# Optimization experiments

Hardware: AMD Instinct MI355X
Metric: run time of the kernel (lower is better)

## Reference

```python
import jax, jax.numpy as jnp
import numpy as np

B, S, H = 4, 2048, 576
NH, NKV, HD = 9, 3, 64
NEG = -1e9


def rotate_half(x):
    x1, x2 = x[..., : HD // 2], x[..., HD // 2 :]
    return jnp.concatenate((-x2, x1), axis=-1)


def setup_inputs() -> dict:
    key = jax.random.key(0)
    ks = jax.random.split(key, 6)
    x = jax.random.normal(ks[0], (B, S, H), dtype=jnp.float32)
    # realistic RoPE tables
    inv_freq = 1.0 / (10000.0 ** (np.arange(0, HD, 2, dtype=np.float32) / HD))
    pos = np.arange(S, dtype=np.float32)
    freqs = np.outer(pos, inv_freq)            # [S, HD//2]
    emb = np.concatenate([freqs, freqs], -1)   # [S, HD]
    cos = jnp.asarray(np.cos(emb), dtype=jnp.float32)
    sin = jnp.asarray(np.sin(emb), dtype=jnp.float32)
    # causal additive mask [1,1,S,S]
    causal = jnp.tril(jnp.ones((S, S), dtype=jnp.bool_))
    mask = jnp.where(causal, 0.0, NEG).astype(jnp.float32)[None, None]
    sc = 1.0 / np.sqrt(H)
    Wq = jax.random.normal(ks[1], (H, NH * HD), dtype=jnp.float32) * sc
    Wk = jax.random.normal(ks[2], (H, NKV * HD), dtype=jnp.float32) * sc
    Wv = jax.random.normal(ks[3], (H, NKV * HD), dtype=jnp.float32) * sc
    Wo = jax.random.normal(ks[4], (NH * HD, H), dtype=jnp.float32) * sc
    return {"x": x, "cos": cos, "sin": sin, "mask": mask,
            "Wq": Wq, "Wk": Wk, "Wv": Wv, "Wo": Wo}


def reference(x, cos, sin, mask, Wq, Wk, Wv, Wo):
    b, s, _ = x.shape
    # projections -> [b, heads, s, hd]
    q = (x @ Wq).reshape(b, s, NH, HD).transpose(0, 2, 1, 3)
    k = (x @ Wk).reshape(b, s, NKV, HD).transpose(0, 2, 1, 3)
    v = (x @ Wv).reshape(b, s, NKV, HD).transpose(0, 2, 1, 3)
    c = cos[None, None]  # [1,1,s,hd]
    sn = sin[None, None]
    q = q * c + rotate_half(q) * sn
    k = k * c + rotate_half(k) * sn
    # GQA: repeat_interleave KV heads to match query heads
    groups = NH // NKV
    k = jnp.repeat(k, groups, axis=1)
    v = jnp.repeat(v, groups, axis=1)
    scores = jnp.einsum("bhqd,bhkd->bhqk", q, k) / np.sqrt(HD)
    scores = scores + mask
    probs = jax.nn.softmax(scores, axis=-1)
    out = jnp.einsum("bhqk,bhkd->bhqd", probs, v)
    out = out.transpose(0, 2, 1, 3).reshape(b, s, NH * HD)
    return out @ Wo
```

## Files before the change

### kernel.cpp

```cpp
#include <hip/hip_runtime.h>
#include <math.h>

typedef __attribute__((ext_vector_type(4))) float f32x4;
typedef __attribute__((ext_vector_type(8))) short short8;
typedef __attribute__((ext_vector_type(8))) __bf16 bf16x8;
typedef __attribute__((ext_vector_type(2))) __bf16 bf16x2;
typedef __attribute__((ext_vector_type(2))) unsigned uint32x2;

#define NB 4
#define NS 2048
#define NHID 576
#define NHEADS 9
#define NKVH 3
#define NHD 64
#define NM (NB * NS)
#define NQKV 960
#define QKS 768
#define NGRP 3
#define QSC 0.18033688f

static __device__ __forceinline__ unsigned short f2bf(float f) {
  union { float f; unsigned u; } v; v.f = f;
  unsigned r = v.u + 0x7FFFu + ((v.u >> 16) & 1u);
  return (unsigned short)(r >> 16);
}
static __device__ __forceinline__ unsigned pk2bf(float a, float b) {
  bf16x2 h;
  h.x = (__bf16)a;
  h.y = (__bf16)b;
  return __builtin_bit_cast(unsigned, h);
}
static __device__ __forceinline__ float bf2f(unsigned short h) {
  union { unsigned u; float f; } v; v.u = ((unsigned)h) << 16;
  return v.f;
}
static __device__ __forceinline__ float fexp2(float x) {
  return __builtin_amdgcn_exp2f(x);
}
static __device__ __forceinline__ f32x4 mfma16(short8 a, short8 b, f32x4 c) {
  return __builtin_amdgcn_mfma_f32_16x16x32_bf16(
      __builtin_bit_cast(bf16x8, a), __builtin_bit_cast(bf16x8, b), c, 0, 0, 0);
}
static __device__ __forceinline__ void gload16(const void* g, void* l) {
  __builtin_amdgcn_global_load_lds(
      (const __attribute__((address_space(1))) void*)g,
      (__attribute__((address_space(3))) void*)l, 16, 0, 0);
}

__global__ __launch_bounds__(256)
void k_prep(const float* __restrict__ x, unsigned short* __restrict__ xb,
            const float* __restrict__ Wq, const float* __restrict__ Wk,
            const float* __restrict__ Wv, const float* __restrict__ Wo,
            unsigned short* __restrict__ wqkvT, unsigned short* __restrict__ woT) {
  __shared__ unsigned short tile[64 * 72];
  int bid = blockIdx.x;
  if (bid < 2304) {
    const int t = bid * 256 + threadIdx.x;
    const f32x4* sp = (const f32x4*)(x + (size_t)t * 8);
    f32x4 a = sp[0], b = sp[1];
    union { short8 v; unsigned short u[8]; } o;
#pragma unroll
    for (int e = 0; e < 4; ++e) { o.u[e] = f2bf(a[e]); o.u[4 + e] = f2bf(b[e]); }
    *(short8*)(xb + (size_t)t * 8) = o.v;
    return;
  }
  bid -= 2304;
  const float* src;
  unsigned short* dst;
  int C, bx, by;
  if (bid < 81) { src = Wq; dst = wqkvT; C = 576; bx = bid % 9; by = bid / 9; }
  else if (bid < 108) { int b2 = bid - 81; src = Wk; dst = wqkvT + 576 * 576; C = 192; bx = b2 % 3; by = b2 / 3; }
  else if (bid < 135) { int b2 = bid - 108; src = Wv; dst = wqkvT + 768 * 576; C = 192; bx = b2 % 3; by = b2 / 3; }
  else { int b2 = bid - 135; src = Wo; dst = woT; C = 576; bx = b2 % 9; by = b2 / 9; }
  const int R = 576;
  const int t = threadIdx.x;
  const int r0 = by * 64, c0 = bx * 64;
  {
    const int rl = t >> 2, cb = (t & 3) * 16;
    const float* sp = src + (size_t)(r0 + rl) * C + c0 + cb;
#pragma unroll
    for (int jj = 0; jj < 4; ++jj) {
      f32x4 v = *(const f32x4*)(sp + jj * 4);
#pragma unroll
      for (int e = 0; e < 4; ++e) tile[rl * 72 + cb + jj * 4 + e] = f2bf(v[e]);
    }
  }
  __syncthreads();
  {
    const int cl = t >> 2, rb = (t & 3) * 16;
    union { short8 v; unsigned short u[8]; } o0, o1;
#pragma unroll
    for (int jj = 0; jj < 8; ++jj) {
      o0.u[jj] = tile[(rb + jj) * 72 + cl];
      o1.u[jj] = tile[(rb + 8 + jj) * 72 + cl];
    }
    unsigned short* dp = dst + (size_t)(c0 + cl) * R + r0 + rb;
    *(short8*)dp = o0.v;
    *(short8*)(dp + 8) = o1.v;
  }
}

template <int MODE>
__global__ __launch_bounds__(256)
void k_gemm_bt(const unsigned short* __restrict__ A,
               const unsigned short* __restrict__ Bt,
               void* __restrict__ Cv,
               unsigned short* __restrict__ vtb,
               const float* __restrict__ cosT,
               const float* __restrict__ sinT,
               const int M, const int N, const int K) {
  __shared__ unsigned short a_lds[2][128 * 64];
  __shared__ unsigned short b_lds[2][128 * 64];
  const int tid = threadIdx.x;
  const int w = tid >> 6, l = tid & 63, g = l >> 4, c = l & 15;
  const int tm = blockIdx.y * 128, tn = blockIdx.x * 128;
  const int wm = w >> 1, wn = w & 1;
  f32x4 acc[4][4] = {};
  const int nk = K >> 6;

#define GSTAGE(k0, half)                                                   \
  {                                                                        \
    _Pragma("unroll")                                                      \
    for (int q = 0; q < 4; ++q) {                                          \
      const int o = q * 4096 + w * 1024 + l * 16;                          \
      const int row = o >> 7;                                              \
      const int wb = (o & 127) ^ ((row & 7) << 4);                         \
      gload16(A + (size_t)(tm + row) * K + (k0) + (wb >> 1),               \
              (void*)(a_lds[half] + ((q * 4096 + w * 1024) >> 1)));        \
      gload16(Bt + (size_t)(tn + row) * K + (k0) + (wb >> 1),              \
              (void*)(b_lds[half] + ((q * 4096 + w * 1024) >> 1)));        \
    }                                                                      \
  }

  GSTAGE(0, 0);

  for (int k = 0; k < nk; ++k) {
    if (k + 1 < nk) {
      GSTAGE((k + 1) << 6, (k + 1) & 1);
      asm volatile("s_waitcnt vmcnt(8)" ::: "memory");
    } else {
      asm volatile("s_waitcnt vmcnt(0)" ::: "memory");
    }
    __builtin_amdgcn_s_barrier();
    __builtin_amdgcn_sched_barrier(0);
    const char* al = (const char*)a_lds[k & 1];
    const char* bl = (const char*)b_lds[k & 1];
#pragma unroll
    for (int dc = 0; dc < 2; ++dc) {
      short8 af[4], bf[4];
#pragma unroll
      for (int mt = 0; mt < 4; ++mt) {
        const int row = wm * 64 + mt * 16 + c;
        const int byt = ((row << 7) + (dc << 6) + (g << 4)) ^ ((row & 7) << 4);
        af[mt] = *(const short8*)(al + byt);
      }
#pragma unroll
      for (int nt = 0; nt < 4; ++nt) {
        const int row = wn * 64 + nt * 16 + c;
        const int byt = ((row << 7) + (dc << 6) + (g << 4)) ^ ((row & 7) << 4);
        bf[nt] = *(const short8*)(bl + byt);
      }
      __builtin_amdgcn_s_setprio(1);
#pragma unroll
      for (int mt = 0; mt < 4; ++mt)
#pragma unroll
        for (int nt = 0; nt < 4; ++nt)
          acc[mt][nt] = mfma16(af[mt], bf[nt], acc[mt][nt]);
      __builtin_amdgcn_s_setprio(0);
    }
    __builtin_amdgcn_sched_barrier(0);
    __builtin_amdgcn_s_barrier();
  }
#undef GSTAGE

  if (MODE == 1) {
#pragma unroll
    for (int mt = 0; mt < 4; ++mt)
#pragma unroll
      for (int nt = 0; nt < 4; ++nt) {
        const int cc = tn + wn * 64 + nt * 16 + c;
        if (cc < N) {
#pragma unroll
          for (int i = 0; i < 4; ++i) {
            const size_t rr = (size_t)(tm + wm * 64 + mt * 16 + 4 * g + i);
            ((float*)Cv)[rr * N + cc] = acc[mt][nt][i];
          }
        }
      }
  } else if (tn < 768) {
    const float qs = (tn + wn * 64) < 576 ? QSC : 1.0f;
    unsigned short* Cp = (unsigned short*)Cv;
#pragma unroll
    for (int mt = 0; mt < 4; ++mt)
#pragma unroll
      for (int i = 0; i < 4; ++i) {
        const int rr = tm + wm * 64 + mt * 16 + 4 * g + i;
        const int s = rr & (NS - 1);
        const float* cb = cosT + (size_t)s * NHD;
        const float* sb = sinT + (size_t)s * NHD;
#pragma unroll
        for (int p = 0; p < 2; ++p) {
          const float cn = cb[p * 16 + c];
          const float sn = sb[p * 16 + c];
          const float lo = acc[mt][p][i];
          const float hi = acc[mt][p + 2][i];
          const size_t base = (size_t)rr * QKS + tn + wn * 64 + p * 16 + c;
          Cp[base] = f2bf((lo * cn - hi * sn) * qs);
          Cp[base + 32] = f2bf((hi * cn + lo * sn) * qs);
        }
      }
  } else {
#pragma unroll
    for (int mt = 0; mt < 4; ++mt)
#pragma unroll
      for (int nt = 0; nt < 4; ++nt) {
        const int cc = tn + wn * 64 + nt * 16 + c;
        if (cc < 960) {
          const int rr0 = tm + wm * 64 + mt * 16 + 4 * g;
          const int bb = rr0 >> 11, ss = rr0 & (NS - 1);
          const int grp = bb * NKVH + ((cc - 768) >> 6);
          const int d = (cc - 768) & 63;
          uint32x2 pk;
          pk.x = pk2bf(acc[mt][nt][0], acc[mt][nt][1]);
          pk.y = pk2bf(acc[mt][nt][2], acc[mt][nt][3]);
          *(uint32x2*)(vtb + (size_t)grp * (NHD * NS) + (size_t)d * NS + ss) = pk;
        }
      }
  }
}

__global__ __launch_bounds__(256)
void k_attn(const unsigned short* __restrict__ qkv,
            const unsigned short* __restrict__ vt,
            unsigned short* __restrict__ ao) {
  __shared__ unsigned short kv_s[2][2][4096];
  __shared__ unsigned short p_s[4][1024];
  const int tid = threadIdx.x;
  const int w = tid >> 6, l = tid & 63, g = l >> 4, c = l & 15;
  const int bh = blockIdx.x;
  const int qt = 31 - (int)blockIdx.y;
  const int b = bh / NHEADS, h = bh - b * NHEADS, kh = h / NGRP;

  const int lr = l >> 3;
  const int swz = ((l & 7) ^ lr) << 4;
  const int r0 = 16 * w + lr;
  const int cs = (c & 7) << 4;

  const char* kp0 = (const char*)(qkv + (size_t)b * NS * QKS + NHEADS * NHD + kh * NHD) +
                    (size_t)r0 * (QKS * 2) + swz;
  const char* kp1 = kp0 + 8 * (QKS * 2);
  const char* vp0 = (const char*)(vt + (size_t)(b * NKVH + kh) * NHD * NS) +
                    (size_t)r0 * (NS * 2) + swz;
  const char* vp1 = vp0 + 8 * (NS * 2);

  const size_t qrow = (size_t)(b * NS + qt * 64 + w * 16 + c) * QKS + h * NHD;
  const short8 qf0 = *(const short8*)(qkv + qrow + g * 8);
  const short8 qf1 = *(const short8*)(qkv + qrow + 32 + g * 8);

  const short8 ones = {0x3F80, 0x3F80, 0x3F80, 0x3F80, 0x3F80, 0x3F80, 0x3F80, 0x3F80};

  f32x4 ot[4] = {};
  f32x4 lacc = {};
  float m = -1e30f;
  const int q_g = qt * 64 + w * 16 + c;

#define STAGE(BUF)                                                \
  {                                                               \
    gload16(kp0, kv_s[BUF][0] + 16 * w * 64);                     \
    gload16(kp1, kv_s[BUF][0] + (16 * w + 8) * 64);               \
    gload16(vp0, kv_s[BUF][1] + 16 * w * 64);                     \
    gload16(vp1, kv_s[BUF][1] + (16 * w + 8) * 64);               \
    kp0 += 64 * (QKS * 2); kp1 += 64 * (QKS * 2);                 \
    vp0 += 128; vp1 += 128;                                       \
  }

#define COMPUTE(BUF, jj)                                                        \
  {                                                                             \
    const char* kl = (const char*)kv_s[BUF][0];                                 \
    const char* vl = (const char*)kv_s[BUF][1];                                 \
    f32x4 st[4] = {};                                                           \
    _Pragma("unroll")                                                           \
    for (int dc = 0; dc < 2; ++dc) {                                            \
      const int col = (dc * 64 + g * 16) ^ cs;                                  \
      const short8 qf = dc ? qf1 : qf0;                                         \
      _Pragma("unroll")                                                         \
      for (int nt = 0; nt < 4; ++nt) {                                          \
        short8 kf = *(const short8*)(kl + (nt * 16 + c) * 128 + col);           \
        st[nt] = mfma16(kf, qf, st[nt]);                                        \
      }                                                                         \
    }                                                                           \
    short8 vf[8];                                                               \
    _Pragma("unroll")                                                           \
    for (int dc = 0; dc < 2; ++dc) {                                            \
      const int col = (dc * 64 + g * 16) ^ cs;                                  \
      _Pragma("unroll")                                                         \
      for (int nt = 0; nt < 4; ++nt)                                            \
        vf[dc * 4 + nt] = *(const short8*)(vl + (nt * 16 + c) * 128 + col);     \
    }                                                                           \
    if ((jj) == qt) {                                                           \
      _Pragma("unroll")                                                         \
      for (int nt = 0; nt < 4; ++nt)                                            \
        _Pragma("unroll")                                                       \
        for (int i = 0; i < 4; ++i) {                                           \
          const int kvg = (jj) * 64 + nt * 16 + 4 * g + i;                      \
          if (kvg > q_g) st[nt][i] = -1e30f;                                    \
        }                                                                       \
    }                                                                           \
    float m0 = fmaxf(fmaxf(st[0][0], st[0][1]), st[0][2]);                      \
    float m1 = fmaxf(fmaxf(st[0][3], st[1][0]), st[1][1]);                      \
    float m2 = fmaxf(fmaxf(st[1][2], st[1][3]), st[2][0]);                      \
    float m3 = fmaxf(fmaxf(st[2][1], st[2][2]), st[2][3]);                      \
    float m4 = fmaxf(fmaxf(st[3][0], st[3][1]), st[3][2]);                      \
    float inmax = fmaxf(fmaxf(fmaxf(m0, m1), fmaxf(m2, m3)),                    \
                        fmaxf(m4, st[3][3]));                                   \
    if (!__all(inmax <= m + 8.0f)) {                                            \
      float pm = fmaxf(inmax, __shfl_xor(inmax, 16));                           \
      pm = fmaxf(pm, __shfl_xor(pm, 32));                                       \
      const float mn = fmaxf(m, pm);                                            \
      const float scl = fexp2(m - mn);                                          \
      m = mn;                                                                   \
      lacc *= scl;                                                              \
      _Pragma("unroll")                                                         \
      for (int nt = 0; nt < 4; ++nt) ot[nt] *= scl;                             \
    }                                                                           \
    {                                                                           \
      char* pw = (char*)p_s[w];                                                 \
      _Pragma("unroll")                                                         \
      for (int nt = 0; nt < 4; ++nt) {                                          \
        float p0 = fexp2(st[nt][0] - m);                                        \
        float p1 = fexp2(st[nt][1] - m);                                        \
        float p2 = fexp2(st[nt][2] - m);                                        \
        float p3 = fexp2(st[nt][3] - m);                                        \
        uint32x2 pk;                                                            \
        pk.x = pk2bf(p0, p1);                                                   \
        pk.y = pk2bf(p2, p3);                                                   \
        *(uint32x2*)(pw + c * 128 + ((nt * 32 + g * 8) ^ cs)) = pk;             \
      }                                                                         \
      _Pragma("unroll")                                                         \
      for (int dc = 0; dc < 2; ++dc) {                                          \
        const int col = (dc * 64 + g * 16) ^ cs;                                \
        short8 pf = *(const short8*)(pw + c * 128 + col);                       \
        lacc = mfma16(ones, pf, lacc);                                          \
        _Pragma("unroll")                                                       \
        for (int nt = 0; nt < 4; ++nt)                                          \
          ot[nt] = mfma16(vf[dc * 4 + nt], pf, ot[nt]);                         \
      }                                                                         \
    }                                                                           \
  }

  STAGE(0);

  for (int j = 0; j <= qt; j += 2) {
    if (j < qt) {
      STAGE(1);
      asm volatile("s_waitcnt vmcnt(4)" ::: "memory");
    } else {
      asm volatile("s_waitcnt vmcnt(0)" ::: "memory");
    }
    __builtin_amdgcn_s_barrier();
    __builtin_amdgcn_sched_barrier(0);
    COMPUTE(0, j);
    __builtin_amdgcn_sched_barrier(0);
    __builtin_amdgcn_s_barrier();
    if (j + 1 > qt) break;
    if (j + 1 < qt) {
      STAGE(0);
      asm volatile("s_waitcnt vmcnt(4)" ::: "memory");
    } else {
      asm volatile("s_waitcnt vmcnt(0)" ::: "memory");
    }
    __builtin_amdgcn_s_barrier();
    __builtin_amdgcn_sched_barrier(0);
    COMPUTE(1, j + 1);
    __builtin_amdgcn_sched_barrier(0);
    __builtin_amdgcn_s_barrier();
  }
#undef STAGE
#undef COMPUTE

  {
    char* ol = (char*)kv_s[0][0];
    const float inv = __builtin_amdgcn_rcpf(lacc[0]);
#pragma unroll
    for (int nt = 0; nt < 4; ++nt) {
      uint32x2 pk;
      pk.x = pk2bf(ot[nt][0] * inv, ot[nt][1] * inv);
      pk.y = pk2bf(ot[nt][2] * inv, ot[nt][3] * inv);
      *(uint32x2*)(ol + (w * 16 + c) * 128 + ((nt * 32 + g * 8) ^ cs)) = pk;
    }
  }
  __syncthreads();
  {
    const char* ol = (const char*)kv_s[0][0];
    const int rr = tid >> 2, cb = tid & 3;
    const int rk = (rr & 7) << 4;
    short8 v0 = *(const short8*)(ol + rr * 128 + ((cb * 32) ^ rk));
    short8 v1 = *(const short8*)(ol + rr * 128 + ((cb * 32 + 16) ^ rk));
    char* aop = (char*)(ao + (size_t)(b * NS + qt * 64 + rr) * NHID + h * NHD + cb * 16);
    *(short8*)aop = v0;
    *(short8*)(aop + 16) = v1;
  }
}

extern "C" void kernel_launch(void* const* d_in, const int* in_sizes, int n_in,
                              void* d_out, int out_size, void* d_ws, size_t ws_size,
                              hipStream_t stream) {
  const float* x = (const float*)d_in[0];
  const float* cosT = (const float*)d_in[1];
  const float* sinT = (const float*)d_in[2];
  const float* Wq = (const float*)d_in[4];
  const float* Wk = (const float*)d_in[5];
  const float* Wv = (const float*)d_in[6];
  const float* Wo = (const float*)d_in[7];

  unsigned short* xb = (unsigned short*)d_ws;
  unsigned short* wqkvT = xb + (size_t)NM * NHID;
  unsigned short* woT = wqkvT + (size_t)NQKV * NHID;
  unsigned short* qkv = woT + (size_t)NHID * NHID;
  unsigned short* vt = qkv + (size_t)NM * QKS;
  unsigned short* ao = xb;

  k_prep<<<dim3(2304 + 216), 256, 0, stream>>>(x, xb, Wq, Wk, Wv, Wo, wqkvT, woT);
  k_gemm_bt<0><<<dim3((NQKV + 127) / 128, NM / 128), 256, 0, stream>>>(
      xb, wqkvT, (void*)qkv, vt, cosT, sinT, NM, NQKV, NHID);
  k_attn<<<dim3(NB * NHEADS, NS / 64), 256, 0, stream>>>(qkv, vt, ao);
  k_gemm_bt<1><<<dim3((NHID + 127) / 128, NM / 128), 256, 0, stream>>>(
      ao, woT, d_out, nullptr, nullptr, nullptr, NM, NHID, NHID);
}
```

Before: 87.42 us.

## Feed softmax probabilities to PV MFMA from registers via 16x16x16 bf16

Drops the per-wave LDS staging buffer for the probability tile. Each lane's packed P values are fed directly as the B operand of 16x16x16 bf16 MFMAs, with V fragments reloaded as 4-element pieces that match that layout. This removes an LDS write/read round trip and its dependency in the inner loop. In exchange it issues twice as many MFMA instructions, each with half the K depth, and does more and narrower LDS reads for V.

New measurement: 89.29 us. 1.02x slower.

```diff
diff --git a/kernel.cpp b/kernel.cpp
--- a/kernel.cpp
+++ b/kernel.cpp
@@ -3,6 +3,7 @@
 
 typedef __attribute__((ext_vector_type(4))) float f32x4;
 typedef __attribute__((ext_vector_type(8))) short short8;
+typedef __attribute__((ext_vector_type(4))) short s16x4;
 typedef __attribute__((ext_vector_type(8))) __bf16 bf16x8;
 typedef __attribute__((ext_vector_type(2))) __bf16 bf16x2;
 typedef __attribute__((ext_vector_type(2))) unsigned uint32x2;
@@ -40,6 +41,19 @@
 static __device__ __forceinline__ f32x4 mfma16(short8 a, short8 b, f32x4 c) {
   return __builtin_amdgcn_mfma_f32_16x16x32_bf16(
       __builtin_bit_cast(bf16x8, a), __builtin_bit_cast(bf16x8, b), c, 0, 0, 0);
+}
+static __device__ __forceinline__ f32x4 mfma16k16(s16x4 a, s16x4 b, f32x4 c) {
+#if defined(__HIP_DEVICE_COMPILE__)
+#if __has_builtin(__builtin_amdgcn_mfma_f32_16x16x16bf16_1k)
+  return __builtin_amdgcn_mfma_f32_16x16x16bf16_1k(a, b, c, 0, 0, 0);
+#else
+  asm volatile("v_mfma_f32_16x16x16_bf16 %0, %1, %2, %0"
+               : "+v"(c) : "v"(a), "v"(b));
+  return c;
+#endif
+#else
+  return c;
+#endif
 }
 static __device__ __forceinline__ void gload16(const void* g, void* l) {
   __builtin_amdgcn_global_load_lds(
@@ -234,7 +248,6 @@
             const unsigned short* __restrict__ vt,
             unsigned short* __restrict__ ao) {
   __shared__ unsigned short kv_s[2][2][4096];
-  __shared__ unsigned short p_s[4][1024];
   const int tid = threadIdx.x;
   const int w = tid >> 6, l = tid & 63, g = l >> 4, c = l & 15;
   const int bh = blockIdx.x;
@@ -257,7 +270,7 @@
   const short8 qf0 = *(const short8*)(qkv + qrow + g * 8);
   const short8 qf1 = *(const short8*)(qkv + qrow + 32 + g * 8);
 
-  const short8 ones = {0x3F80, 0x3F80, 0x3F80, 0x3F80, 0x3F80, 0x3F80, 0x3F80, 0x3F80};
+  const s16x4 ones4 = {0x3F80, 0x3F80, 0x3F80, 0x3F80};
 
   f32x4 ot[4] = {};
   f32x4 lacc = {};
@@ -289,14 +302,13 @@
         st[nt] = mfma16(kf, qf, st[nt]);                                        \
       }                                                                         \
     }                                                                           \
-    short8 vf[8];                                                               \
+    s16x4 vq[16];             \
     _Pragma("unroll")                                                           \
-    for (int dc = 0; dc < 2; ++dc) {                                            \
-      const int col = (dc * 64 + g * 16) ^ cs;                                  \
+    for (int nt = 0; nt < 4; ++nt)                                              \
       _Pragma("unroll")                                                         \
-      for (int nt = 0; nt < 4; ++nt)                                            \
-        vf[dc * 4 + nt] = *(const short8*)(vl + (nt * 16 + c) * 128 + col);     \
-    }                                                                           \
+      for (int kb = 0; kb < 4; ++kb)                                            \
+        vq[nt * 4 + kb] = *(const s16x4*)(vl + (nt * 16 + c) * 128 +            \
+                                          ((kb * 32 + g * 8) ^ cs));            \
     if ((jj) == qt) {                                                           \
       _Pragma("unroll")                                                         \
       for (int nt = 0; nt < 4; ++nt)                                            \
@@ -324,26 +336,26 @@
       for (int nt = 0; nt < 4; ++nt) ot[nt] *= scl;                             \
     }                                                                           \
     {                                                                           \
-      char* pw = (char*)p_s[w];                                                 \
+      union PBu { unsigned u[2]; s16x4 v; };                                    \
+      PBu pb0, pb1, pb2, pb3;                                                   \
+      pb0.u[0] = pk2bf(fexp2(st[0][0] - m), fexp2(st[0][1] - m));               \
+      pb0.u[1] = pk2bf(fexp2(st[0][2] - m), fexp2(st[0][3] - m));               \
+      pb1.u[0] = pk2bf(fexp2(st[1][0] - m), fexp2(st[1][1] - m));               \
+      pb1.u[1] = pk2bf(fexp2(st[1][2] - m), fexp2(st[1][3] - m));               \
+      pb2.u[0] = pk2bf(fexp2(st[2][0] - m), fexp2(st[2][1] - m));               \
+      pb2.u[1] = pk2bf(fexp2(st[2][2] - m), fexp2(st[2][3] - m));               \
+      pb3.u[0] = pk2bf(fexp2(st[3][0] - m), fexp2(st[3][1] - m));               \
+      pb3.u[1] = pk2bf(fexp2(st[3][2] - m), fexp2(st[3][3] - m));               \
+      lacc = mfma16k16(ones4, pb0.v, lacc);                                     \
+      lacc = mfma16k16(ones4, pb1.v, lacc);                                     \
+      lacc = mfma16k16(ones4, pb2.v, lacc);                                     \
+      lacc = mfma16k16(ones4, pb3.v, lacc);                                     \
       _Pragma("unroll")                                                         \
       for (int nt = 0; nt < 4; ++nt) {                                          \
-        float p0 = fexp2(st[nt][0] - m);                                        \
-        float p1 = fexp2(st[nt][1] - m);                                        \
-        float p2 = fexp2(st[nt][2] - m);                                        \
-        float p3 = fexp2(st[nt][3] - m);                                        \
-        uint32x2 pk;                                                            \
-        pk.x = pk2bf(p0, p1);                                                   \
-        pk.y = pk2bf(p2, p3);                                                   \
-        *(uint32x2*)(pw + c * 128 + ((nt * 32 + g * 8) ^ cs)) = pk;             \
-      }                                                                         \
-      _Pragma("unroll")                                                         \
-      for (int dc = 0; dc < 2; ++dc) {                                          \
-        const int col = (dc * 64 + g * 16) ^ cs;                                \
-        short8 pf = *(const short8*)(pw + c * 128 + col);                       \
-        lacc = mfma16(ones, pf, lacc);                                          \
-        _Pragma("unroll")                                                       \
-        for (int nt = 0; nt < 4; ++nt)                                          \
-          ot[nt] = mfma16(vf[dc * 4 + nt], pf, ot[nt]);                         \
+        ot[nt] = mfma16k16(vq[nt * 4 + 0], pb0.v, ot[nt]);                      \
+        ot[nt] = mfma16k16(vq[nt * 4 + 1], pb1.v, ot[nt]);                      \
+        ot[nt] = mfma16k16(vq[nt * 4 + 2], pb2.v, ot[nt]);                      \
+        ot[nt] = mfma16k16(vq[nt * 4 + 3], pb3.v, ot[nt]);                      \
       }                                                                         \
     }                                                                           \
   }
```
